# Kernel tuning notes

Measured on AMD Instinct MI355X. Metric: run time of the kernel, lower is better.

Reference implementation:

```python
import jax, jax.numpy as jnp
import numpy as np

NUM_CLUSTERS = 256
NUM_HEADS = 16
DIM_PER_HEAD = 64
NGRAM_VOCAB = 768 * 256
NGRAM_EMB_DIM = 8
DECAY = 0.999
EPS_PQ = 1e-06
LN_EPS = 1e-05


def _first_primes_after(start, count):
    primes = []
    n = start
    while len(primes) < count:
        n += 1
        if all(n % p for p in range(2, int(n ** 0.5) + 1)):
            primes.append(n)
    return np.array(primes, dtype=np.int64)

# first NUM_HEADS primes in (NGRAM_VOCAB, 2*NGRAM_VOCAB), matching sympy.primerange
_PRIMES = _first_primes_after(NGRAM_VOCAB, NUM_HEADS)


def _layer_norm(v, scale, bias):
    # reduction over last axis; per-(head, feature) scale/bias (flax feature_axes=(-2,-1))
    mu = jnp.mean(v, axis=-1, keepdims=True)
    var = jnp.var(v, axis=-1, keepdims=True)
    return (v - mu) * jax.lax.rsqrt(var + LN_EPS) * scale + bias


def setup_inputs() -> dict:
    key = jax.random.key(0)
    k1, k2, k3 = jax.random.split(key, 3)
    B, L = 4, 4096
    x = jax.random.normal(k1, (B, L, NUM_HEADS * DIM_PER_HEAD), dtype=jnp.float32)
    means = jax.random.normal(k2, (NUM_HEADS, NUM_CLUSTERS, DIM_PER_HEAD), dtype=jnp.float32)
    embed_table = jax.random.normal(k3, (NGRAM_VOCAB * NUM_HEADS, NGRAM_EMB_DIM), dtype=jnp.float32)
    ln_x_scale = jnp.ones((NUM_HEADS, DIM_PER_HEAD), dtype=jnp.float32)
    ln_x_bias = jnp.zeros((NUM_HEADS, DIM_PER_HEAD), dtype=jnp.float32)
    ln_y_scale = jnp.ones((NUM_HEADS, NGRAM_EMB_DIM), dtype=jnp.float32)
    ln_y_bias = jnp.zeros((NUM_HEADS, NGRAM_EMB_DIM), dtype=jnp.float32)
    return {"x": x, "means": means, "embed_table": embed_table,
            "ln_x_scale": ln_x_scale, "ln_x_bias": ln_x_bias,
            "ln_y_scale": ln_y_scale, "ln_y_bias": ln_y_bias}


def reference(x, means, embed_table, ln_x_scale, ln_x_bias, ln_y_scale, ln_y_bias):
    B, L, HD = x.shape
    H, K, D = means.shape
    E = NGRAM_EMB_DIM
    xh = x.reshape(B, L, H, D)

    # --- ProductQuantization: squared-distance cluster assignment ---
    x_sq = jnp.sum(jnp.square(xh), axis=-1, keepdims=True)            # [B,L,H,1]
    m_sq = jnp.sum(jnp.square(means), axis=-1)[None, None]            # [1,1,H,K]
    dists = x_sq + m_sq - 2.0 * jnp.einsum('blhd,hkd->blhk', xh, means)
    cluster_ids = jnp.argmin(dists, axis=-1).astype(jnp.int32)        # [B,L,H]

    # --- EMA means update (train-mode side effect) ---
    one_hot = jax.nn.one_hot(cluster_ids, K, dtype=xh.dtype)          # [B,L,H,K]
    counts = jnp.sum(one_hot, axis=(0, 1))                            # [H,K]
    sum_x = jnp.einsum('blhk,blhd->hkd', one_hot, xh)                 # [H,K,D]
    means_x = sum_x / (EPS_PQ + counts[..., None])
    new_means = (1.0 - DECAY) * means_x + DECAY * means

    # --- bigram ids: ids[t] + ids[t-1] * vocab ---
    prev = jnp.pad(cluster_ids[:, :-1], ((0, 0), (1, 0), (0, 0)))     # [B,L,H]
    ngram_cluster_ids = cluster_ids + prev * NUM_CLUSTERS             # < K*K, fits int32

    # --- multi-way hash per head ---
    head = jnp.arange(H, dtype=jnp.int32)                             # [H]
    primes = jnp.asarray(_PRIMES, dtype=jnp.int32)                    # [H]
    hashed = (ngram_cluster_ids * (head + 1) + (head + 1)) % primes % NGRAM_VOCAB
    ngram_ids = hashed + NGRAM_VOCAB * head                           # [B,L,H]

    # --- ngram embedding gather + per-head LayerNorms + concat ---
    y = embed_table[ngram_ids]                                        # [B,L,H,E]
    normed_x = _layer_norm(xh, ln_x_scale, ln_x_bias)
    normed_y = _layer_norm(y, ln_y_scale, ln_y_bias)
    out = jnp.concatenate((normed_x[..., : D - E], normed_y), axis=-1)
    out = out.reshape(B, L, H * D)
    return out, new_means
```

## Files before the change

kernel.cpp:

```cpp
#include <hip/hip_runtime.h>
#include <cstdint>
#include <cstddef>

#define NH 16
#define ND 64
#define NK 256
#define NE 8
#define NV 196608
#define NBL 16384
#define MS 68

struct Primes { int p[NH]; };

__global__ __launch_bounds__(256) void k_pq(
    const float* __restrict__ x, const float* __restrict__ means,
    const float* __restrict__ lnxs, const float* __restrict__ lnxb,
    float* __restrict__ out, uint8_t* __restrict__ cids,
    float* __restrict__ gsum, int* __restrict__ gcnt)
{
  __shared__ float sm[NK * MS];
  __shared__ float smsq[NK];
  __shared__ int   scnt[NK];
  __shared__ float ssc[ND], sbi[ND];

  const int tid = threadIdx.x;
  const int h   = blockIdx.y;

  {
    const float4* mr = (const float4*)(means + ((size_t)h * NK + tid) * ND);
    float4* dst = (float4*)(sm + tid * MS);
    float msq = 0.f;
#pragma unroll
    for (int i = 0; i < 16; ++i) {
      float4 v = mr[i];
      dst[i] = v;
      msq += v.x * v.x + v.y * v.y + v.z * v.z + v.w * v.w;
    }
    smsq[tid] = msq;
  }
  if (tid < ND) { ssc[tid] = lnxs[h * ND + tid]; sbi[tid] = lnxb[h * ND + tid]; }
  __syncthreads();

  const int g = blockIdx.x * 256 + tid;
  const float4* xr4 = (const float4*)(x + ((size_t)g * NH + h) * ND);
  float4 xr[16];
  float xsq = 0.f, xsum = 0.f;
#pragma unroll
  for (int i = 0; i < 16; ++i) {
    float4 v = xr4[i];
    xr[i] = v;
    xsq  += v.x * v.x + v.y * v.y + v.z * v.z + v.w * v.w;
    xsum += v.x + v.y + v.z + v.w;
  }

  float best = 3.4e38f;
  int bk = 0;
#pragma unroll 2
  for (int k = 0; k < NK; ++k) {
    const float4* m4 = (const float4*)(sm + k * MS);
    float ax = 0.f, ay = 0.f, az = 0.f, aw = 0.f;
#pragma unroll
    for (int i = 0; i < 16; ++i) {
      float4 m = m4[i];
      ax = fmaf(xr[i].x, m.x, ax);
      ay = fmaf(xr[i].y, m.y, ay);
      az = fmaf(xr[i].z, m.z, az);
      aw = fmaf(xr[i].w, m.w, aw);
    }
    float dot  = (ax + ay) + (az + aw);
    float dist = (xsq + smsq[k]) - 2.0f * dot;
    if (dist < best) { best = dist; bk = k; }
  }
  cids[(size_t)g * NH + h] = (uint8_t)bk;

  {
    float mu  = xsum * (1.f / 64.f);
    float var = xsq * (1.f / 64.f) - mu * mu;
    float rs  = rsqrtf(var + 1e-5f);
    float* orow = out + ((size_t)g * NH + h) * ND;
#pragma unroll
    for (int i = 0; i < 14; ++i) {
      float4 v = xr[i];
      float4 o;
      o.x = (v.x - mu) * rs * ssc[4 * i + 0] + sbi[4 * i + 0];
      o.y = (v.y - mu) * rs * ssc[4 * i + 1] + sbi[4 * i + 1];
      o.z = (v.z - mu) * rs * ssc[4 * i + 2] + sbi[4 * i + 2];
      o.w = (v.w - mu) * rs * ssc[4 * i + 3] + sbi[4 * i + 3];
      ((float4*)orow)[i] = o;
    }
  }

  __syncthreads();
#pragma unroll
  for (int d = 0; d < ND; ++d) sm[d * NK + tid] = 0.f;
  scnt[tid] = 0;
  __syncthreads();

  atomicAdd(&scnt[bk], 1);
#pragma unroll
  for (int i = 0; i < 16; ++i) {
    atomicAdd(&sm[(4 * i + 0) * NK + bk], xr[i].x);
    atomicAdd(&sm[(4 * i + 1) * NK + bk], xr[i].y);
    atomicAdd(&sm[(4 * i + 2) * NK + bk], xr[i].z);
    atomicAdd(&sm[(4 * i + 3) * NK + bk], xr[i].w);
  }
  __syncthreads();

  const int cnt = scnt[tid];
  if (cnt > 0) atomicAdd(&gcnt[h * NK + tid], cnt);
  const bool act = cnt > 0;
#pragma unroll 4
  for (int d = 0; d < ND; ++d) {
    if (act) atomicAdd(&gsum[((size_t)h * ND + d) * NK + tid], sm[d * NK + tid]);
  }
}

__global__ __launch_bounds__(256) void k_ngram(
    const uint8_t* __restrict__ cids, const float* __restrict__ embed,
    const float* __restrict__ lys, const float* __restrict__ lyb,
    float* __restrict__ out, Primes pr)
{
  const int i = blockIdx.x * 256 + threadIdx.x;
  const int h = i & 15;
  const int g = i >> 4;
  const int l = g & 4095;

  int cid  = (int)cids[i];
  int prev = (l == 0) ? 0 : (int)cids[i - NH];
  int ng   = cid + (prev << 8);
  int hp1  = h + 1;
  int v    = ng * hp1 + hp1;
  const int p = pr.p[h];
  while (v >= p) v -= p;
  if (v >= NV) v -= NV;

  const float4* e4 = (const float4*)(embed + ((size_t)(v + NV * h)) * NE);
  float4 y0 = e4[0], y1 = e4[1];

  float s = ((y0.x + y0.y) + (y0.z + y0.w)) + ((y1.x + y1.y) + (y1.z + y1.w));
  float mu = s * 0.125f;
  float q = y0.x * y0.x + y0.y * y0.y + y0.z * y0.z + y0.w * y0.w
          + y1.x * y1.x + y1.y * y1.y + y1.z * y1.z + y1.w * y1.w;
  float var = q * 0.125f - mu * mu;
  float rs  = rsqrtf(var + 1e-5f);

  const float* sc = lys + h * NE;
  const float* bi = lyb + h * NE;
  float4 o0, o1;
  o0.x = (y0.x - mu) * rs * sc[0] + bi[0];
  o0.y = (y0.y - mu) * rs * sc[1] + bi[1];
  o0.z = (y0.z - mu) * rs * sc[2] + bi[2];
  o0.w = (y0.w - mu) * rs * sc[3] + bi[3];
  o1.x = (y1.x - mu) * rs * sc[4] + bi[4];
  o1.y = (y1.y - mu) * rs * sc[5] + bi[5];
  o1.z = (y1.z - mu) * rs * sc[6] + bi[6];
  o1.w = (y1.w - mu) * rs * sc[7] + bi[7];

  float4* orow = (float4*)(out + ((size_t)g * NH + h) * ND + 56);
  orow[0] = o0;
  orow[1] = o1;
}

__global__ __launch_bounds__(256) void k_means(
    const float* __restrict__ means, const float* __restrict__ gsum,
    const int* __restrict__ gcnt, float* __restrict__ newm)
{
  const int i = blockIdx.x * 256 + threadIdx.x;
  const int d = i & 63;
  const int k = (i >> 6) & 255;
  const int h = i >> 14;
  float cnt = (float)gcnt[h * NK + k];
  float sx  = gsum[((size_t)h * ND + d) * NK + k];
  float mx  = sx / (1e-6f + cnt);
  const float omd = (float)(1.0 - 0.999);
  newm[i] = omd * mx + 0.999f * means[i];
}

extern "C" void kernel_launch(void* const* d_in, const int* in_sizes, int n_in,
                              void* d_out, int out_size, void* d_ws, size_t ws_size,
                              hipStream_t stream)
{
  const float* x     = (const float*)d_in[0];
  const float* means = (const float*)d_in[1];
  const float* embed = (const float*)d_in[2];
  const float* lnxs  = (const float*)d_in[3];
  const float* lnxb  = (const float*)d_in[4];
  const float* lys   = (const float*)d_in[5];
  const float* lyb   = (const float*)d_in[6];

  float* out  = (float*)d_out;
  float* newm = out + (size_t)NBL * NH * ND;

  float*   gsum = (float*)d_ws;
  int*     gcnt = (int*)((char*)d_ws + (size_t)NH * NK * ND * 4);
  uint8_t* cids = (uint8_t*)((char*)d_ws + (size_t)NH * NK * ND * 4 + (size_t)NH * NK * 4);

  hipMemsetAsync(d_ws, 0, (size_t)NH * NK * ND * 4 + (size_t)NH * NK * 4, stream);

  Primes pr;
  {
    int n = NV, c = 0;
    while (c < NH) {
      ++n;
      bool isp = true;
      for (int q = 2; (long long)q * q <= n; ++q)
        if (n % q == 0) { isp = false; break; }
      if (isp) pr.p[c++] = n;
    }
  }

  dim3 g1(NBL / 256, NH);
  k_pq<<<g1, 256, 0, stream>>>(x, means, lnxs, lnxb, out, cids, gsum, gcnt);
  k_ngram<<<(NBL * NH) / 256, 256, 0, stream>>>(cids, embed, lys, lyb, out, pr);
  k_means<<<(NH * NK * ND) / 256, 256, 0, stream>>>(means, gsum, gcnt, newm);
}
```

Before: 276.6 us.

## Register-tile distance computation with 64-token blocks and split-K argmin

Replaces the one-token-per-thread distance loop with a register-blocked tile: each thread computes 4 tokens by 16 clusters, with x and means staged in shared memory in two halves along the feature dimension. The argmin is finished by a shuffle reduction across 16 lanes. Blocks now cover 64 tokens instead of 256, and the shared cluster-sum accumulator is padded to avoid bank conflicts. The aim is better FLOP-to-shared-load reuse, at the cost of four times more blocks, each doing its own global atomics for the means update.

```diff
diff --git a/kernel.cpp b/kernel.cpp
--- a/kernel.cpp
+++ b/kernel.cpp
@@ -8,101 +8,164 @@
 #define NE 8
 #define NV 196608
 #define NBL 16384
-#define MS 68
+#define TOK 64
+#define ACC_STRIDE 257
 
 struct Primes { int p[NH]; };
 
-__global__ __launch_bounds__(256) void k_pq(
+__global__ __launch_bounds__(256, 2) void k_pq(
     const float* __restrict__ x, const float* __restrict__ means,
     const float* __restrict__ lnxs, const float* __restrict__ lnxb,
     float* __restrict__ out, uint8_t* __restrict__ cids,
     float* __restrict__ gsum, int* __restrict__ gcnt)
 {
-  __shared__ float sm[NK * MS];
-  __shared__ float smsq[NK];
-  __shared__ int   scnt[NK];
-  __shared__ float ssc[ND], sbi[ND];
-
-  const int tid = threadIdx.x;
-  const int h   = blockIdx.y;
-
-  {
-    const float4* mr = (const float4*)(means + ((size_t)h * NK + tid) * ND);
-    float4* dst = (float4*)(sm + tid * MS);
-    float msq = 0.f;
+  __shared__ __align__(16) float smem[16704];
+  float4* sx4   = (float4*)smem;
+  float4* sm4   = (float4*)(smem + 4096);
+  float*  smsq  = smem + 12288;
+  float*  lnsc  = smem + 12544;
+  float*  lnbi  = smem + 12608;
+  float*  accum = smem;
+  int*    scnt  = (int*)(smem + 16448);
+
+  const int tid     = threadIdx.x;
+  const int h       = blockIdx.y;
+  const int g0      = blockIdx.x * TOK;
+  const int tok_row = tid >> 4;
+  const int cl_col  = tid & 15;
+
+  {
+    const int t = tid >> 2, part = tid & 3;
+    const float4* xs = (const float4*)(x + ((size_t)(g0 + t) * NH + h) * ND) + part * 4;
+#pragma unroll
+    for (int j = 0; j < 4; ++j) sx4[(part * 4 + j) * TOK + t] = xs[j];
+  }
+  if (tid < ND) { lnsc[tid] = lnxs[h * ND + tid]; lnbi[tid] = lnxb[h * ND + tid]; }
+  scnt[tid] = 0;
+
+  float acc[4][16];
+#pragma unroll
+  for (int j = 0; j < 4; ++j)
+#pragma unroll
+    for (int i = 0; i < 16; ++i) acc[j][i] = 0.f;
+
+  for (int half = 0; half < 2; ++half) {
+    if (half) __syncthreads();
+    {
+      const float4* msrc = (const float4*)(means + ((size_t)h * NK + tid) * ND + half * 32);
+      float mp = 0.f;
+#pragma unroll
+      for (int i = 0; i < 8; ++i) {
+        float4 v = msrc[i];
+        sm4[i * NK + tid] = v;
+        mp += v.x * v.x + v.y * v.y + v.z * v.z + v.w * v.w;
+      }
+      if (half == 0) smsq[tid] = mp; else smsq[tid] += mp;
+    }
+    __syncthreads();
+
+#pragma unroll 2
+    for (int dc = 0; dc < 8; ++dc) {
+      float4 xv[4];
+#pragma unroll
+      for (int j = 0; j < 4; ++j) xv[j] = sx4[(half * 8 + dc) * TOK + tok_row * 4 + j];
+#pragma unroll
+      for (int i = 0; i < 16; ++i) {
+        float4 mv = sm4[dc * NK + i * 16 + cl_col];
+#pragma unroll
+        for (int j = 0; j < 4; ++j) {
+          float a = acc[j][i];
+          a = fmaf(xv[j].x, mv.x, a);
+          a = fmaf(xv[j].y, mv.y, a);
+          a = fmaf(xv[j].z, mv.z, a);
+          a = fmaf(xv[j].w, mv.w, a);
+          acc[j][i] = a;
+        }
+      }
+    }
+  }
+
+  int bk[4];
+  {
+    float bv[4]; int bi[4];
+#pragma unroll
+    for (int j = 0; j < 4; ++j) { bv[j] = 3.4e38f; bi[j] = 0; }
 #pragma unroll
     for (int i = 0; i < 16; ++i) {
-      float4 v = mr[i];
-      dst[i] = v;
-      msq += v.x * v.x + v.y * v.y + v.z * v.z + v.w * v.w;
-    }
-    smsq[tid] = msq;
-  }
-  if (tid < ND) { ssc[tid] = lnxs[h * ND + tid]; sbi[tid] = lnxb[h * ND + tid]; }
+      const int c = i * 16 + cl_col;
+      const float mq = smsq[c];
+#pragma unroll
+      for (int j = 0; j < 4; ++j) {
+        float d = mq - 2.0f * acc[j][i];
+        if (d < bv[j]) { bv[j] = d; bi[j] = c; }
+      }
+    }
+#pragma unroll
+    for (int j = 0; j < 4; ++j) {
+      float v = bv[j]; int c = bi[j];
+#pragma unroll
+      for (int m = 1; m < 16; m <<= 1) {
+        float ov = __shfl_xor(v, m);
+        int   oc = __shfl_xor(c, m);
+        if (ov < v || (ov == v && oc < c)) { v = ov; c = oc; }
+      }
+      bk[j] = c;
+    }
+    if (cl_col == 0) {
+#pragma unroll
+      for (int j = 0; j < 4; ++j) {
+        const int t = tok_row * 4 + j;
+        cids[(size_t)(g0 + t) * NH + h] = (uint8_t)bk[j];
+        atomicAdd(&scnt[bk[j]], 1);
+      }
+    }
+  }
+
+  {
+    const int t = tid >> 2, q = tid & 3;
+    float4 v[4];
+    float s = 0.f, sq = 0.f;
+#pragma unroll
+    for (int j = 0; j < 4; ++j) {
+      v[j] = sx4[(q * 4 + j) * TOK + t];
+      s  += v[j].x + v[j].y + v[j].z + v[j].w;
+      sq += v[j].x * v[j].x + v[j].y * v[j].y + v[j].z * v[j].z + v[j].w * v[j].w;
+    }
+    s  += __shfl_xor(s, 1);  sq += __shfl_xor(sq, 1);
+    s  += __shfl_xor(s, 2);  sq += __shfl_xor(sq, 2);
+    float mu  = s * (1.f / 64.f);
+    float var = sq * (1.f / 64.f) - mu * mu;
+    float rs  = rsqrtf(var + 1e-5f);
+    float* orow = out + ((size_t)(g0 + t) * NH + h) * ND;
+#pragma unroll
+    for (int j = 0; j < 4; ++j) {
+      const int dc = q * 4 + j;
+      if (dc < 14) {
+        float4 o;
+        o.x = (v[j].x - mu) * rs * lnsc[dc * 4 + 0] + lnbi[dc * 4 + 0];
+        o.y = (v[j].y - mu) * rs * lnsc[dc * 4 + 1] + lnbi[dc * 4 + 1];
+        o.z = (v[j].z - mu) * rs * lnsc[dc * 4 + 2] + lnbi[dc * 4 + 2];
+        o.w = (v[j].w - mu) * rs * lnsc[dc * 4 + 3] + lnbi[dc * 4 + 3];
+        ((float4*)orow)[dc] = o;
+      }
+    }
+  }
+
+  float4 xr[4];
+#pragma unroll
+  for (int j = 0; j < 4; ++j) xr[j] = sx4[cl_col * TOK + tok_row * 4 + j];
+
   __syncthreads();
-
-  const int g = blockIdx.x * 256 + tid;
-  const float4* xr4 = (const float4*)(x + ((size_t)g * NH + h) * ND);
-  float4 xr[16];
-  float xsq = 0.f, xsum = 0.f;
-#pragma unroll
-  for (int i = 0; i < 16; ++i) {
-    float4 v = xr4[i];
-    xr[i] = v;
-    xsq  += v.x * v.x + v.y * v.y + v.z * v.z + v.w * v.w;
-    xsum += v.x + v.y + v.z + v.w;
-  }
-
-  float best = 3.4e38f;
-  int bk = 0;
-#pragma unroll 2
-  for (int k = 0; k < NK; ++k) {
-    const float4* m4 = (const float4*)(sm + k * MS);
-    float ax = 0.f, ay = 0.f, az = 0.f, aw = 0.f;
-#pragma unroll
-    for (int i = 0; i < 16; ++i) {
-      float4 m = m4[i];
-      ax = fmaf(xr[i].x, m.x, ax);
-      ay = fmaf(xr[i].y, m.y, ay);
-      az = fmaf(xr[i].z, m.z, az);
-      aw = fmaf(xr[i].w, m.w, aw);
-    }
-    float dot  = (ax + ay) + (az + aw);
-    float dist = (xsq + smsq[k]) - 2.0f * dot;
-    if (dist < best) { best = dist; bk = k; }
-  }
-  cids[(size_t)g * NH + h] = (uint8_t)bk;
-
-  {
-    float mu  = xsum * (1.f / 64.f);
-    float var = xsq * (1.f / 64.f) - mu * mu;
-    float rs  = rsqrtf(var + 1e-5f);
-    float* orow = out + ((size_t)g * NH + h) * ND;
-#pragma unroll
-    for (int i = 0; i < 14; ++i) {
-      float4 v = xr[i];
-      float4 o;
-      o.x = (v.x - mu) * rs * ssc[4 * i + 0] + sbi[4 * i + 0];
-      o.y = (v.y - mu) * rs * ssc[4 * i + 1] + sbi[4 * i + 1];
-      o.z = (v.z - mu) * rs * ssc[4 * i + 2] + sbi[4 * i + 2];
-      o.w = (v.w - mu) * rs * ssc[4 * i + 3] + sbi[4 * i + 3];
-      ((float4*)orow)[i] = o;
-    }
-  }
-
+  for (int idx = tid; idx < 64 * ACC_STRIDE; idx += 256) accum[idx] = 0.f;
   __syncthreads();
-#pragma unroll
-  for (int d = 0; d < ND; ++d) sm[d * NK + tid] = 0.f;
-  scnt[tid] = 0;
-  __syncthreads();
-
-  atomicAdd(&scnt[bk], 1);
-#pragma unroll
-  for (int i = 0; i < 16; ++i) {
-    atomicAdd(&sm[(4 * i + 0) * NK + bk], xr[i].x);
-    atomicAdd(&sm[(4 * i + 1) * NK + bk], xr[i].y);
-    atomicAdd(&sm[(4 * i + 2) * NK + bk], xr[i].z);
-    atomicAdd(&sm[(4 * i + 3) * NK + bk], xr[i].w);
+
+#pragma unroll
+  for (int j = 0; j < 4; ++j) {
+    const int b = bk[j];
+    atomicAdd(&accum[(cl_col * 4 + 0) * ACC_STRIDE + b], xr[j].x);
+    atomicAdd(&accum[(cl_col * 4 + 1) * ACC_STRIDE + b], xr[j].y);
+    atomicAdd(&accum[(cl_col * 4 + 2) * ACC_STRIDE + b], xr[j].z);
+    atomicAdd(&accum[(cl_col * 4 + 3) * ACC_STRIDE + b], xr[j].w);
   }
   __syncthreads();
 
@@ -111,7 +174,7 @@
   const bool act = cnt > 0;
 #pragma unroll 4
   for (int d = 0; d < ND; ++d) {
-    if (act) atomicAdd(&gsum[((size_t)h * ND + d) * NK + tid], sm[d * NK + tid]);
+    if (act) atomicAdd(&gsum[((size_t)h * ND + d) * NK + tid], accum[d * ACC_STRIDE + tid]);
   }
 }
 
@@ -172,8 +235,7 @@
   float cnt = (float)gcnt[h * NK + k];
   float sx  = gsum[((size_t)h * ND + d) * NK + k];
   float mx  = sx / (1e-6f + cnt);
-  const float omd = (float)(1.0 - 0.999);
-  newm[i] = omd * mx + 0.999f * means[i];
+  newm[i] = 0.001f * mx + 0.999f * means[i];
 }
 
 extern "C" void kernel_launch(void* const* d_in, const int* in_sizes, int n_in,
@@ -209,7 +271,7 @@
     }
   }
 
-  dim3 g1(NBL / 256, NH);
+  dim3 g1(NBL / TOK, NH);
   k_pq<<<g1, 256, 0, stream>>>(x, means, lnxs, lnxb, out, cids, gsum, gcnt);
   k_ngram<<<(NBL * NH) / 256, 256, 0, stream>>>(cids, embed, lys, lyb, out, pr);
   k_means<<<(NH * NK * ND) / 256, 256, 0, stream>>>(means, gsum, gcnt, newm);
```

Result: slower. 339.7 us (+22.8%).

## Process 512 tokens per PQ block and flush only active cluster sums

Applied to the files above, without the earlier changes.

The PQ kernel now uses 512-thread blocks covering 512 tokens, so each means tile loaded into shared memory is reused across twice as many tokens, and the per-block global atomic flush is amortized. It drops the constant x_sq term from the argmin distance, pads the shared accumulator stride to 257 to reduce bank conflicts, and builds a list of active clusters so global atomics cover only clusters that received tokens. gsum is relaid out as [H,K,D], making the flush and the means-update reads contiguous. Risks: fewer blocks (512 total), higher register pressure under launch_bounds(512,2), and floating-point ordering changes in the sums.

```diff
diff --git a/kernel.cpp b/kernel.cpp
--- a/kernel.cpp
+++ b/kernel.cpp
@@ -8,49 +8,62 @@
 #define NE 8
 #define NV 196608
 #define NBL 16384
+#define TOK 512
 #define MS 68
+#define ACC_STRIDE 257
 
 struct Primes { int p[NH]; };
 
-__global__ __launch_bounds__(256) void k_pq(
+__global__ __launch_bounds__(512, 2) void k_pq(
     const float* __restrict__ x, const float* __restrict__ means,
     const float* __restrict__ lnxs, const float* __restrict__ lnxb,
     float* __restrict__ out, uint8_t* __restrict__ cids,
     float* __restrict__ gsum, int* __restrict__ gcnt)
 {
-  __shared__ float sm[NK * MS];
-  __shared__ float smsq[NK];
-  __shared__ int   scnt[NK];
-  __shared__ float ssc[ND], sbi[ND];
+  __shared__ __align__(16) float smem[18561];
+  float*  sm      = smem;
+  float*  smsq2   = smem + 17408;
+  int*    scnt    = (int*)(smem + 17920);
+  int*    sactive = (int*)(smem + 18176);
+  int*    snact   = (int*)(smem + 18432);
+  float*  lnsc    = smem + 18433;
+  float*  lnbi    = smem + 18497;
+  float*  accum   = smem;
 
   const int tid = threadIdx.x;
   const int h   = blockIdx.y;
-
-  {
-    const float4* mr = (const float4*)(means + ((size_t)h * NK + tid) * ND);
-    float4* dst = (float4*)(sm + tid * MS);
-    float msq = 0.f;
-#pragma unroll
-    for (int i = 0; i < 16; ++i) {
-      float4 v = mr[i];
-      dst[i] = v;
-      msq += v.x * v.x + v.y * v.y + v.z * v.z + v.w * v.w;
-    }
-    smsq[tid] = msq;
-  }
-  if (tid < ND) { ssc[tid] = lnxs[h * ND + tid]; sbi[tid] = lnxb[h * ND + tid]; }
-  __syncthreads();
-
-  const int g = blockIdx.x * 256 + tid;
-  const float4* xr4 = (const float4*)(x + ((size_t)g * NH + h) * ND);
+  const int g0  = blockIdx.x * TOK;
+  const int g   = g0 + tid;
+
+  {
+    const int cl = tid >> 1, hf = tid & 1;
+    const float4* src = (const float4*)(means + ((size_t)h * NK + cl) * ND + hf * 32);
+    float4* dst = (float4*)(sm + cl * MS + hf * 32);
+    float mp = 0.f;
+#pragma unroll
+    for (int j = 0; j < 8; ++j) {
+      float4 v = src[j];
+      dst[j] = v;
+      mp += v.x * v.x + v.y * v.y + v.z * v.z + v.w * v.w;
+    }
+    smsq2[hf * NK + cl] = mp;
+  }
+  if (tid < ND) { lnsc[tid] = lnxs[h * ND + tid]; lnbi[tid] = lnxb[h * ND + tid]; }
+  if (tid < NK) scnt[tid] = 0;
+  if (tid == 0) *snact = 0;
+  __syncthreads();
+  if (tid < NK) smsq2[tid] += smsq2[NK + tid];
+  __syncthreads();
+
+  const float4* xg = (const float4*)(x + ((size_t)g * NH + h) * ND);
   float4 xr[16];
-  float xsq = 0.f, xsum = 0.f;
+  float xsum = 0.f, xsq = 0.f;
 #pragma unroll
   for (int i = 0; i < 16; ++i) {
-    float4 v = xr4[i];
+    float4 v = xg[i];
     xr[i] = v;
+    xsum += v.x + v.y + v.z + v.w;
     xsq  += v.x * v.x + v.y * v.y + v.z * v.z + v.w * v.w;
-    xsum += v.x + v.y + v.z + v.w;
   }
 
   float best = 3.4e38f;
@@ -68,10 +81,32 @@
       aw = fmaf(xr[i].w, m.w, aw);
     }
     float dot  = (ax + ay) + (az + aw);
-    float dist = (xsq + smsq[k]) - 2.0f * dot;
+    float dist = smsq2[k] - 2.0f * dot;
     if (dist < best) { best = dist; bk = k; }
   }
   cids[(size_t)g * NH + h] = (uint8_t)bk;
+  atomicAdd(&scnt[bk], 1);
+
+  __syncthreads();
+
+  for (int idx = tid; idx < ND * ACC_STRIDE; idx += 512) accum[idx] = 0.f;
+  if (tid < NK) {
+    const int cnt = scnt[tid];
+    if (cnt > 0) {
+      int p = atomicAdd(snact, 1);
+      sactive[p] = tid;
+      atomicAdd(&gcnt[h * NK + tid], cnt);
+    }
+  }
+  __syncthreads();
+
+#pragma unroll
+  for (int i = 0; i < 16; ++i) {
+    atomicAdd(&accum[(4 * i + 0) * ACC_STRIDE + bk], xr[i].x);
+    atomicAdd(&accum[(4 * i + 1) * ACC_STRIDE + bk], xr[i].y);
+    atomicAdd(&accum[(4 * i + 2) * ACC_STRIDE + bk], xr[i].z);
+    atomicAdd(&accum[(4 * i + 3) * ACC_STRIDE + bk], xr[i].w);
+  }
 
   {
     float mu  = xsum * (1.f / 64.f);
@@ -82,36 +117,22 @@
     for (int i = 0; i < 14; ++i) {
       float4 v = xr[i];
       float4 o;
-      o.x = (v.x - mu) * rs * ssc[4 * i + 0] + sbi[4 * i + 0];
-      o.y = (v.y - mu) * rs * ssc[4 * i + 1] + sbi[4 * i + 1];
-      o.z = (v.z - mu) * rs * ssc[4 * i + 2] + sbi[4 * i + 2];
-      o.w = (v.w - mu) * rs * ssc[4 * i + 3] + sbi[4 * i + 3];
+      o.x = (v.x - mu) * rs * lnsc[4 * i + 0] + lnbi[4 * i + 0];
+      o.y = (v.y - mu) * rs * lnsc[4 * i + 1] + lnbi[4 * i + 1];
+      o.z = (v.z - mu) * rs * lnsc[4 * i + 2] + lnbi[4 * i + 2];
+      o.w = (v.w - mu) * rs * lnsc[4 * i + 3] + lnbi[4 * i + 3];
       ((float4*)orow)[i] = o;
     }
   }
-
-  __syncthreads();
-#pragma unroll
-  for (int d = 0; d < ND; ++d) sm[d * NK + tid] = 0.f;
-  scnt[tid] = 0;
-  __syncthreads();
-
-  atomicAdd(&scnt[bk], 1);
-#pragma unroll
-  for (int i = 0; i < 16; ++i) {
-    atomicAdd(&sm[(4 * i + 0) * NK + bk], xr[i].x);
-    atomicAdd(&sm[(4 * i + 1) * NK + bk], xr[i].y);
-    atomicAdd(&sm[(4 * i + 2) * NK + bk], xr[i].z);
-    atomicAdd(&sm[(4 * i + 3) * NK + bk], xr[i].w);
-  }
-  __syncthreads();
-
-  const int cnt = scnt[tid];
-  if (cnt > 0) atomicAdd(&gcnt[h * NK + tid], cnt);
-  const bool act = cnt > 0;
-#pragma unroll 4
-  for (int d = 0; d < ND; ++d) {
-    if (act) atomicAdd(&gsum[((size_t)h * ND + d) * NK + tid], sm[d * NK + tid]);
+  __syncthreads();
+
+  {
+    const int d = tid & 63, grp = tid >> 6;
+    const int nact = *snact;
+    for (int a = grp; a < nact; a += 8) {
+      const int cl = sactive[a];
+      atomicAdd(&gsum[(((size_t)h << 8) + cl) * ND + d], accum[d * ACC_STRIDE + cl]);
+    }
   }
 }
 
@@ -166,14 +187,9 @@
     const int* __restrict__ gcnt, float* __restrict__ newm)
 {
   const int i = blockIdx.x * 256 + threadIdx.x;
-  const int d = i & 63;
-  const int k = (i >> 6) & 255;
-  const int h = i >> 14;
-  float cnt = (float)gcnt[h * NK + k];
-  float sx  = gsum[((size_t)h * ND + d) * NK + k];
-  float mx  = sx / (1e-6f + cnt);
-  const float omd = (float)(1.0 - 0.999);
-  newm[i] = omd * mx + 0.999f * means[i];
+  float cnt = (float)gcnt[i >> 6];
+  float mx  = gsum[i] / (1e-6f + cnt);
+  newm[i] = 0.001f * mx + 0.999f * means[i];
 }
 
 extern "C" void kernel_launch(void* const* d_in, const int* in_sizes, int n_in,
@@ -209,8 +225,8 @@
     }
   }
 
-  dim3 g1(NBL / 256, NH);
-  k_pq<<<g1, 256, 0, stream>>>(x, means, lnxs, lnxb, out, cids, gsum, gcnt);
+  dim3 g1(NBL / TOK, NH);
+  k_pq<<<g1, 512, 0, stream>>>(x, means, lnxs, lnxb, out, cids, gsum, gcnt);
   k_ngram<<<(NBL * NH) / 256, 256, 0, stream>>>(cids, embed, lys, lyb, out, pr);
   k_means<<<(NH * NK * ND) / 256, 256, 0, stream>>>(means, gsum, gcnt, newm);
 }
```

New measurement: 421.6 us. +52.4%, slower.
